# Optimization experiments

Measured on AMD Instinct MI355X. Metric: run time of the kernel, lower is better.

## Reference

```python
import jax, jax.numpy as jnp
import numpy as np

WS = 8          # window_size
POOL = 7        # int(sqrt(agent_num=49)) -> AdaptiveAvgPool1d output size


def _pool_matrix(L, p):
    """Averaging matrix [L, p] replicating torch AdaptiveAvgPool1d(L -> p)."""
    starts = np.floor(np.arange(p) * L / p).astype(int)
    ends = np.ceil((np.arange(p) + 1) * L / p).astype(int)
    P = np.zeros((L, p), dtype=np.float32)
    for i in range(p):
        P[starts[i]:ends[i], i] = 1.0 / (ends[i] - starts[i])
    return jnp.asarray(P)


def setup_inputs() -> dict:
    key = jax.random.key(0)
    ks = jax.random.split(key, 4)
    B, C, H, W = 8, 96, 192, 192
    s = 1.0 / np.sqrt(C)
    return {
        "x": jax.random.normal(ks[0], (B, C, H, W), jnp.float32),
        "Wv": jax.random.normal(ks[1], (C, C), jnp.float32) * s,
        "bv": jnp.zeros((C,), jnp.float32),
        "Wq": jax.random.normal(ks[2], (C, C), jnp.float32) * s,
        "bq": jnp.zeros((C,), jnp.float32),
        "Wk": jax.random.normal(ks[3], (C, C), jnp.float32) * s,
        "bk": jnp.zeros((C,), jnp.float32),
    }


def _conv1x1(x, Wt, b):
    # Conv2d(dim, dim, 1): weight [out, in]
    return jnp.einsum('bchw,oc->bohw', x, Wt) + b[None, :, None, None]


def reference(x, Wv, bv, Wq, bq, Wk, bk):
    B, C, H, W = x.shape
    ws = WS
    nh, nw = H // ws, W // ws
    L = ws * ws  # tokens per window (64)

    v = _conv1x1(x, Wv, bv)
    q = _conv1x1(x, Wq, bq)
    k = _conv1x1(x, Wk, bk)

    def win(t):  # b c (h dh) (w dw) -> (b h w) (dh dw) c
        t = t.reshape(B, C, nh, ws, nw, ws)
        return t.transpose(0, 2, 4, 3, 5, 1).reshape(B * nh * nw, L, C)

    vw, qw, kw = win(v), win(q), win(k)  # (N, 64, C) each

    # agent tokens: adaptive avg pool over the 64 in-window positions -> 7
    P = _pool_matrix(L, POOL)
    agent = jnp.einsum('nlc,lp->npc', qw, P)  # (N, 7, C)

    # agent attention (attn_drop = 0 -> identity)
    a_attn = jax.nn.softmax(jnp.einsum('npc,nlc->npl', agent, kw), axis=-1)
    agent_v = jnp.einsum('npl,nlc->npc', a_attn, vw)            # (N, 7, C)
    q_attn = jax.nn.softmax(jnp.einsum('nlc,npc->nlp', qw, agent), axis=-1)
    f = jnp.einsum('nlp,npc->nlc', q_attn, agent_v)             # (N, 64, C)

    # (b h w) (dh dw) c -> b c (h dh) (w dw)
    out = f.reshape(B, nh, nw, ws, ws, C).transpose(0, 5, 1, 3, 2, 4)
    return out.reshape(B, C, H, W)
```

## Files before the change

kernel.cpp:

```cpp
#include <hip/hip_runtime.h>


constexpr int C_   = 96;
constexpr int Wimg = 192;
constexpr int HWp  = 192 * 192;
constexpr int NWIN = 24;
constexpr int Pp   = 7;

typedef __attribute__((ext_vector_type(8))) __bf16 bf16x8;
typedef __attribute__((ext_vector_type(4))) __bf16 bf16x4;
typedef __attribute__((ext_vector_type(8))) short  short8;
typedef __attribute__((ext_vector_type(4))) float  f32x4;
union frag_u { short8 s; bf16x8 b; };

constexpr int XWS   = 0;
constexpr int XWLC  = 12288;
constexpr int R1    = 24768;
constexpr int R2    = 31168;
constexpr int QATB  = 37568;
constexpr int SMEMB = 39872;

constexpr int WS_FRAG_BYTE = 18944 * 4;
constexpr int WS_WV_BYTE   = WS_FRAG_BYTE + 84 * 1024;


__device__ __forceinline__ void bar() {
    asm volatile("s_waitcnt lgkmcnt(0)" ::: "memory");
    __builtin_amdgcn_s_barrier();
}

__device__ __forceinline__ void hilo8(const float4 a, const float4 b,
                                      frag_u& H, frag_u& L) {
    float v[8] = {a.x, a.y, a.z, a.w, b.x, b.y, b.z, b.w};
    #pragma unroll
    for (int j = 0; j < 8; ++j) {
        const __bf16 h = (__bf16)v[j];
        H.b[j] = h;
        L.b[j] = (__bf16)(v[j] - (float)h);
    }
}

__device__ __forceinline__ short8 xws_fragA(const unsigned char* S, int mt, int ks, int lane) {
    const int c  = mt * 16 + (lane & 15);
    const int l2 = ks * 64 + ((lane >> 4) << 4);
    return *reinterpret_cast<const short8*>(S + XWS + c * 128 + (l2 ^ ((c & 7) << 4)));
}


__global__ void precompute_mats(const float* __restrict__ Wq,
                                const float* __restrict__ Wk,
                                float* __restrict__ Mk,
                                float* __restrict__ Mq)
{
    const int c  = blockIdx.x;
    const int cp = threadIdx.x;
    float ak = 0.f, aq = 0.f;
    for (int a = 0; a < C_; ++a) {
        const float wq = Wq[a * C_ + c];
        ak = fmaf(wq, Wk[a * C_ + cp], ak);
        aq = fmaf(wq, Wq[a * C_ + cp], aq);
    }
    Mk[c * C_ + cp] = ak;
    Mq[c * C_ + cp] = aq;
}

__global__ void precompute_vecs(const float* __restrict__ Wq,
                                const float* __restrict__ Wk,
                                const float* __restrict__ bq,
                                const float* __restrict__ bk,
                                float* __restrict__ uk,  float* __restrict__ uq,
                                float* __restrict__ bk2, float* __restrict__ bq2,
                                float* __restrict__ scal)
{
    const int c = threadIdx.x;
    float a_uk = 0.f, a_uq = 0.f, a_bk2 = 0.f, a_bq2 = 0.f;
    for (int a = 0; a < C_; ++a) {
        const float wqc = Wq[a * C_ + c];
        a_uk  = fmaf(wqc, bk[a], a_uk);
        a_uq  = fmaf(wqc, bq[a], a_uq);
        a_bk2 = fmaf(bq[a], Wk[a * C_ + c], a_bk2);
        a_bq2 = fmaf(bq[a], Wq[a * C_ + c], a_bq2);
    }
    uk[c] = a_uk; uq[c] = a_uq; bk2[c] = a_bk2; bq2[c] = a_bq2;
    if (c == 0) {
        float sk = 0.f, sq = 0.f;
        for (int a = 0; a < C_; ++a) { sk += bq[a] * bk[a]; sq += bq[a] * bq[a]; }
        scal[0] = sk; scal[1] = sq;
    }
}

__global__ void precompute_frags(const float* __restrict__ ws,
                                 const float* __restrict__ Wv,
                                 unsigned char* __restrict__ wsb)
{
    const int bid = blockIdx.x, lane = threadIdx.x;
    short8 o;
    if (bid < 84) {
        const int hl = bid & 1, ks = (bid >> 1) % 3, nt = (bid / 6) % 7, mat = bid / 42;
        const float* M = ws + (mat ? 9216 : 0);
        const float* u = ws + (mat ? 18528 : 18432);
        const int col = nt * 16 + (lane & 15);
        #pragma unroll
        for (int j = 0; j < 8; ++j) {
            const int k = ks * 32 + (lane >> 4) * 8 + j;
            const float raw = (col < 96) ? M[k * 96 + col] : ((col == 96) ? u[k] : 0.f);
            const __bf16 hi = (__bf16)raw;
            union { __bf16 h; short s; } cv;
            cv.h = hl ? (__bf16)(raw - (float)hi) : hi;
            o[j] = cv.s;
        }
        *reinterpret_cast<short8*>(wsb + WS_FRAG_BYTE + bid * 1024 + lane * 16) = o;
    } else {
        const int wb = bid - 84;
        const int hl = wb & 1, ks = (wb >> 1) % 3, mt = wb / 6;
        const int row = mt * 16 + (lane & 15);
        #pragma unroll
        for (int j = 0; j < 8; ++j) {
            const int c = ks * 32 + (lane >> 4) * 8 + j;
            const float raw = Wv[row * 96 + c];
            const __bf16 hi = (__bf16)raw;
            union { __bf16 h; short s; } cv;
            cv.h = hl ? (__bf16)(raw - (float)hi) : hi;
            o[j] = cv.s;
        }
        *reinterpret_cast<short8*>(wsb + WS_WV_BYTE + wb * 1024 + lane * 16) = o;
    }
}

#define LOADPAIR(dstH, dstL, tab, slot_h) do {                                        \
    (dstH).s = *reinterpret_cast<const short8*>((tab) + (slot_h) * 1024 + (lane << 4));      \
    (dstL).s = *reinterpret_cast<const short8*>((tab) + ((slot_h) + 1) * 1024 + (lane << 4));\
} while (0)


__global__ __launch_bounds__(256, 4) void camixer_main(
    const float* __restrict__ x,
    const float* __restrict__ bv,
    const float* __restrict__ bk2,
    const float* __restrict__ bq2,
    const float* __restrict__ scal,
    const unsigned char* __restrict__ mfrag,
    const unsigned char* __restrict__ wvfrag,
    float* __restrict__ out)
{
    __shared__ __align__(16) unsigned char S[SMEMB];
    float* xpf  = (float*)(S + R1);
    float* Lraw = (float*)(S + R1);
    float* xvf  = (float*)(S + R1);
    float* gkq  = (float*)(S + R2);
    float* avT  = (float*)(S + R2);
    float* qat  = (float*)(S + QATB);

    const int t = threadIdx.x;
    const int lane = t & 63, w = t >> 6;
    const int wid = ((blockIdx.x & 7) * 576) + (blockIdx.x >> 3);
    const int b  = wid / (NWIN * NWIN);
    const int r  = wid % (NWIN * NWIN);
    const int h0 = (r / NWIN) * 8;
    const int w0 = (r % NWIN) * 8;
    const int base = b * C_ * HWp + h0 * Wimg + w0;
    const float scal0 = scal[0], scal1 = scal[1];

    frag_u B0h[3], B0l[3];
    LOADPAIR(B0h[0], B0l[0], mfrag, (w * 3 + 0) * 2);
    LOADPAIR(B0h[1], B0l[1], mfrag, (w * 3 + 1) * 2);
    LOADPAIR(B0h[2], B0l[2], mfrag, (w * 3 + 2) * 2);

    {
        const float4* x4 = reinterpret_cast<const float4*>(x);
        #pragma unroll
        for (int rr = 0; rr < 2; ++rr) {
            const int idx = t + (rr << 8);
            if (idx < 384) {
                const int dw4 = idx & 1;
                const int dh  = (idx >> 1) & 7;
                const int c4  = idx >> 4;
                const int c0 = c4 * 4, l0 = dh * 8 + dw4 * 4;
                __bf16 bf[4][4];
                #pragma unroll
                for (int j = 0; j < 4; ++j) {
                    const float4 v = x4[(base + (c0 + j) * HWp + dh * Wimg + dw4 * 4) >> 2];
                    bf[j][0] = (__bf16)v.x; bf[j][1] = (__bf16)v.y;
                    bf[j][2] = (__bf16)v.z; bf[j][3] = (__bf16)v.w;
                }
                #pragma unroll
                for (int j = 0; j < 4; ++j) {
                    const int c = c0 + j;
                    bf16x4 d = {bf[j][0], bf[j][1], bf[j][2], bf[j][3]};
                    *reinterpret_cast<bf16x4*>(S + XWS + c * 128 + ((l0 * 2) ^ ((c & 7) << 4))) = d;
                }
                #pragma unroll
                for (int i = 0; i < 4; ++i) {
                    const int l = l0 + i;
                    const int s = (c0 >> 5) * 4 + (l >> 4);
                    const int quad = (l & 15) + ((c0 >> 3) & 3) * 16;
                    bf16x4 d = {bf[0][i], bf[1][i], bf[2][i], bf[3][i]};
                    *reinterpret_cast<bf16x4*>(S + XWLC + s * 1040 + quad * 16 + (c0 & 7) * 2) = d;
                }
            }
        }
    }
    bar();

    {
        frag_u PAh[2], PAl[2];
        {
            const int p = lane & 15, kb = lane >> 4;
            const __bf16 PH = (__bf16)0.1f;
            const __bf16 PL = (__bf16)(0.1f - (float)PH);
            const int sp = (p < 7) ? ((p << 6) / 7) : 1000;
            #pragma unroll
            for (int ks = 0; ks < 2; ++ks)
                #pragma unroll
                for (int j = 0; j < 8; ++j) {
                    const int l = ks * 32 + kb * 8 + j;
                    const bool in = (l >= sp) && (l < sp + 10);
                    PAh[ks].b[j] = in ? PH : (__bf16)0.f;
                    PAl[ks].b[j] = in ? PL : (__bf16)0.f;
                }
        }
        #pragma unroll
        for (int rnd = 0; rnd < 2; ++rnd) {
            const int nt = rnd ? (4 + w) : w;
            if (rnd == 0 || w < 2) {
                f32x4 acc = {0.f, 0.f, 0.f, 0.f};
                #pragma unroll
                for (int ks = 0; ks < 2; ++ks) {
                    frag_u B;
                    B.s = xws_fragA(S, nt, ks, lane);
                    acc = __builtin_amdgcn_mfma_f32_16x16x32_bf16(PAh[ks].b, B.b, acc, 0, 0, 0);
                    acc = __builtin_amdgcn_mfma_f32_16x16x32_bf16(PAl[ks].b, B.b, acc, 0, 0, 0);
                }
                const int cc = nt * 16 + (lane & 15);
                #pragma unroll
                for (int rr = 0; rr < 4; ++rr)
                    xpf[((lane >> 4) * 4 + rr) * 100 + cc] = acc[rr];
            }
        }
    }
    bar();

    {
        frag_u Ah[3], Al[3];
        #pragma unroll
        for (int ks = 0; ks < 3; ++ks) {
            const int off = (lane & 15) * 100 + ks * 32 + (lane >> 4) * 8;
            hilo8(*reinterpret_cast<const float4*>(&xpf[off]),
                  *reinterpret_cast<const float4*>(&xpf[off + 4]), Ah[ks], Al[ks]);
        }

        #define G0TILE(TT, BH, BL) do {                                               \
            const int tt_ = (TT);                                                     \
            const int mat_ = (tt_ >= 7) ? 1 : 0;                                      \
            const int nt_  = tt_ - 7 * mat_;                                          \
            f32x4 acc = {0.f, 0.f, 0.f, 0.f};                                         \
            acc = __builtin_amdgcn_mfma_f32_16x16x32_bf16(Ah[0].b, BH[0].b, acc, 0,0,0); \
            acc = __builtin_amdgcn_mfma_f32_16x16x32_bf16(Ah[0].b, BL[0].b, acc, 0,0,0); \
            acc = __builtin_amdgcn_mfma_f32_16x16x32_bf16(Al[0].b, BH[0].b, acc, 0,0,0); \
            acc = __builtin_amdgcn_mfma_f32_16x16x32_bf16(Ah[1].b, BH[1].b, acc, 0,0,0); \
            acc = __builtin_amdgcn_mfma_f32_16x16x32_bf16(Ah[1].b, BL[1].b, acc, 0,0,0); \
            acc = __builtin_amdgcn_mfma_f32_16x16x32_bf16(Al[1].b, BH[1].b, acc, 0,0,0); \
            acc = __builtin_amdgcn_mfma_f32_16x16x32_bf16(Ah[2].b, BH[2].b, acc, 0,0,0); \
            acc = __builtin_amdgcn_mfma_f32_16x16x32_bf16(Ah[2].b, BL[2].b, acc, 0,0,0); \
            acc = __builtin_amdgcn_mfma_f32_16x16x32_bf16(Al[2].b, BH[2].b, acc, 0,0,0); \
            const int row0_ = (lane >> 4) * 4;                                        \
            if (nt_ < 6) {                                                            \
                const int cc_ = nt_ * 16 + (lane & 15);                               \
                const float b2v_ = (mat_ ? bq2 : bk2)[cc_];                           \
                _Pragma("unroll")                                                     \
                for (int rr = 0; rr < 4; ++rr) {                                      \
                    const int rw_ = row0_ + rr;                                       \
                    if (rw_ < 8) gkq[(rw_ + 8 * mat_) * 100 + cc_] = acc[rr] + b2v_;  \
                }                                                                     \
            } else if ((lane & 15) == 0) {                                            \
                _Pragma("unroll")                                                     \
                for (int rr = 0; rr < 4; ++rr) {                                      \
                    const int rw_ = row0_ + rr;                                       \
                    if (rw_ < 8) gkq[(rw_ + 8 * mat_) * 100 + 96] = acc[rr];          \
                }                                                                     \
            }                                                                         \
        } while (0)

        frag_u B1h[3], B1l[3], B2h[3], B2l[3], B3h[3], B3l[3];
        LOADPAIR(B1h[0], B1l[0], mfrag, (((w + 4) % 7 + 7 * ((w + 4) / 7)) * 3 + 0) * 2);
        LOADPAIR(B1h[1], B1l[1], mfrag, ((w + 4) * 3 + 1) * 2);
        LOADPAIR(B1h[2], B1l[2], mfrag, ((w + 4) * 3 + 2) * 2);
        G0TILE(w, B0h, B0l);
        LOADPAIR(B2h[0], B2l[0], mfrag, ((w + 8) * 3 + 0) * 2);
        LOADPAIR(B2h[1], B2l[1], mfrag, ((w + 8) * 3 + 1) * 2);
        LOADPAIR(B2h[2], B2l[2], mfrag, ((w + 8) * 3 + 2) * 2);
        G0TILE(w + 4, B1h, B1l);
        if (w < 2) {
            LOADPAIR(B3h[0], B3l[0], mfrag, ((w + 12) * 3 + 0) * 2);
            LOADPAIR(B3h[1], B3l[1], mfrag, ((w + 12) * 3 + 1) * 2);
            LOADPAIR(B3h[2], B3l[2], mfrag, ((w + 12) * 3 + 2) * 2);
        }
        G0TILE(w + 8, B2h, B2l);
        if (w < 2) G0TILE(w + 12, B3h, B3l);
        #undef G0TILE
    }
    bar();

    {
        frag_u B[3];
        #pragma unroll
        for (int ks = 0; ks < 3; ++ks)
            B[ks].s = *reinterpret_cast<const short8*>(S + XWLC + (ks * 4 + w) * 1040 + (lane << 4));
        frag_u Ah[3], Al[3];
        #pragma unroll
        for (int ks = 0; ks < 3; ++ks) {
            const int off = (lane & 15) * 100 + ks * 32 + (lane >> 4) * 8;
            hilo8(*reinterpret_cast<const float4*>(&gkq[off]),
                  *reinterpret_cast<const float4*>(&gkq[off + 4]), Ah[ks], Al[ks]);
        }
        f32x4 acc = {0.f, 0.f, 0.f, 0.f};
        #pragma unroll
        for (int ks = 0; ks < 3; ++ks) {
            acc = __builtin_amdgcn_mfma_f32_16x16x32_bf16(Ah[ks].b, B[ks].b, acc, 0, 0, 0);
            acc = __builtin_amdgcn_mfma_f32_16x16x32_bf16(Al[ks].b, B[ks].b, acc, 0, 0, 0);
        }
        const int colL = w * 16 + (lane & 15);
        #pragma unroll
        for (int rr = 0; rr < 4; ++rr) {
            const int pr = (lane >> 4) * 4 + rr;
            const float bias = gkq[pr * 100 + 96] + (pr < 8 ? scal0 : scal1);
            Lraw[pr * 66 + colL] = acc[rr] + bias;
        }
    }
    bar();

    if (w < 3) {
        #pragma unroll
        for (int rr = 0; rr < 2; ++rr) {
            const int pp = w + 3 * rr;
            const float v = Lraw[pp * 66 + lane];
            float mx = v;
            #pragma unroll
            for (int off = 32; off; off >>= 1) mx = fmaxf(mx, __shfl_xor(mx, off));
            const float e = __expf(v - mx);
            float s = e;
            #pragma unroll
            for (int off = 32; off; off >>= 1) s += __shfl_xor(s, off);
            const float a = e / s;
            const __bf16 hb = (__bf16)a;
            const __bf16 lb = (__bf16)(a - (float)hb);
            const int ks = lane >> 5;
            const int off_b = ((pp + 16 * ((lane >> 3) & 3)) << 4) + ((lane & 7) << 1);
            *reinterpret_cast<__bf16*>(S + R2 + (ks << 10) + off_b) = hb;
            *reinterpret_cast<__bf16*>(S + R2 + ((2 + ks) << 10) + off_b) = lb;
        }
    } else {
        {
            const int pp = 6;
            const float v = Lraw[pp * 66 + lane];
            float mx = v;
            #pragma unroll
            for (int off = 32; off; off >>= 1) mx = fmaxf(mx, __shfl_xor(mx, off));
            const float e = __expf(v - mx);
            float s = e;
            #pragma unroll
            for (int off = 32; off; off >>= 1) s += __shfl_xor(s, off);
            const float a = e / s;
            const __bf16 hb = (__bf16)a;
            const __bf16 lb = (__bf16)(a - (float)hb);
            const int ks = lane >> 5;
            const int off_b = ((pp + 16 * ((lane >> 3) & 3)) << 4) + ((lane & 7) << 1);
            *reinterpret_cast<__bf16*>(S + R2 + (ks << 10) + off_b) = hb;
            *reinterpret_cast<__bf16*>(S + R2 + ((2 + ks) << 10) + off_b) = lb;
        }
        float vv[Pp];
        float mx = -1e30f;
        #pragma unroll
        for (int p = 0; p < Pp; ++p) { vv[p] = Lraw[(8 + p) * 66 + lane]; mx = fmaxf(mx, vv[p]); }
        float s = 0.f;
        #pragma unroll
        for (int p = 0; p < Pp; ++p) { vv[p] = __expf(vv[p] - mx); s += vv[p]; }
        const float inv = 1.f / s;
        #pragma unroll
        for (int p = 0; p < Pp; ++p) qat[lane * 9 + p] = vv[p] * inv;
    }
    bar();

    frag_u V0h[3], V0l[3], V1h[3], V1l[3];
    {
        LOADPAIR(V0h[0], V0l[0], wvfrag, (w * 3 + 0) * 2);
        LOADPAIR(V0h[1], V0l[1], wvfrag, (w * 3 + 1) * 2);
        LOADPAIR(V0h[2], V0l[2], wvfrag, (w * 3 + 2) * 2);
        if (w < 2) {
            LOADPAIR(V1h[0], V1l[0], wvfrag, ((4 + w) * 3 + 0) * 2);
            LOADPAIR(V1h[1], V1l[1], wvfrag, ((4 + w) * 3 + 1) * 2);
            LOADPAIR(V1h[2], V1l[2], wvfrag, ((4 + w) * 3 + 2) * 2);
        }

        frag_u Bh[2], Bl[2];
        #pragma unroll
        for (int ks = 0; ks < 2; ++ks) {
            Bh[ks].s = *reinterpret_cast<const short8*>(S + R2 + (ks << 10) + (lane << 4));
            Bl[ks].s = *reinterpret_cast<const short8*>(S + R2 + ((2 + ks) << 10) + (lane << 4));
        }
        const int mt0 = (w < 2) ? w * 2 : (w + 2);
        const int nmt = (w < 2) ? 2 : 1;
        for (int m = 0; m < nmt; ++m) {
            const int mt = mt0 + m;
            f32x4 acc = {0.f, 0.f, 0.f, 0.f};
            #pragma unroll
            for (int ks = 0; ks < 2; ++ks) {
                frag_u A;
                A.s = xws_fragA(S, mt, ks, lane);
                acc = __builtin_amdgcn_mfma_f32_16x16x32_bf16(A.b, Bh[ks].b, acc, 0, 0, 0);
                acc = __builtin_amdgcn_mfma_f32_16x16x32_bf16(A.b, Bl[ks].b, acc, 0, 0, 0);
            }
            const int p = lane & 15;
            const int c0 = mt * 16 + (lane >> 4) * 4;
            *reinterpret_cast<f32x4*>(&xvf[p * 100 + c0]) = acc;
        }
    }
    bar();

    {
        frag_u Bh[3], Bl[3];
        #pragma unroll
        for (int ks = 0; ks < 3; ++ks) {
            const int off = (lane & 15) * 100 + ks * 32 + (lane >> 4) * 8;
            hilo8(*reinterpret_cast<const float4*>(&xvf[off]),
                  *reinterpret_cast<const float4*>(&xvf[off + 4]), Bh[ks], Bl[ks]);
        }
        #define G3TILE(MT, VH, VL) do {                                               \
            f32x4 acc = {0.f, 0.f, 0.f, 0.f};                                         \
            acc = __builtin_amdgcn_mfma_f32_16x16x32_bf16(VH[0].b, Bh[0].b, acc, 0,0,0); \
            acc = __builtin_amdgcn_mfma_f32_16x16x32_bf16(VH[0].b, Bl[0].b, acc, 0,0,0); \
            acc = __builtin_amdgcn_mfma_f32_16x16x32_bf16(VL[0].b, Bh[0].b, acc, 0,0,0); \
            acc = __builtin_amdgcn_mfma_f32_16x16x32_bf16(VH[1].b, Bh[1].b, acc, 0,0,0); \
            acc = __builtin_amdgcn_mfma_f32_16x16x32_bf16(VH[1].b, Bl[1].b, acc, 0,0,0); \
            acc = __builtin_amdgcn_mfma_f32_16x16x32_bf16(VL[1].b, Bh[1].b, acc, 0,0,0); \
            acc = __builtin_amdgcn_mfma_f32_16x16x32_bf16(VH[2].b, Bh[2].b, acc, 0,0,0); \
            acc = __builtin_amdgcn_mfma_f32_16x16x32_bf16(VH[2].b, Bl[2].b, acc, 0,0,0); \
            acc = __builtin_amdgcn_mfma_f32_16x16x32_bf16(VL[2].b, Bh[2].b, acc, 0,0,0); \
            if ((lane & 15) < 8) {                                                    \
                _Pragma("unroll")                                                     \
                for (int rr = 0; rr < 4; ++rr) {                                      \
                    const int o_ = (MT) * 16 + (lane >> 4) * 4 + rr;                  \
                    avT[o_ * 8 + (lane & 15)] = acc[rr] + bv[o_];                     \
                }                                                                     \
            }                                                                         \
        } while (0)
        G3TILE(w, V0h, V0l);
        if (w < 2) G3TILE(4 + w, V1h, V1l);
        #undef G3TILE
    }
    bar();

    {
        float qa[Pp];
        #pragma unroll
        for (int p = 0; p < Pp; ++p) qa[p] = qat[lane * 9 + p];
        const int dh = lane >> 3, dw = lane & 7;
        const int obase = b * C_ * HWp + (h0 + dh) * Wimg + (w0 + dw);
        #pragma unroll 4
        for (int j = 0; j < 24; ++j) {
            const int o = w + 4 * j;
            const float4 a0 = *reinterpret_cast<const float4*>(&avT[o * 8]);
            const float4 a1 = *reinterpret_cast<const float4*>(&avT[o * 8 + 4]);
            float acc = qa[0] * a0.x;
            acc = fmaf(qa[1], a0.y, acc);
            acc = fmaf(qa[2], a0.z, acc);
            acc = fmaf(qa[3], a0.w, acc);
            acc = fmaf(qa[4], a1.x, acc);
            acc = fmaf(qa[5], a1.y, acc);
            acc = fmaf(qa[6], a1.z, acc);
            out[obase + o * HWp] = acc;
        }
    }
}


extern "C" void kernel_launch(void* const* d_in, const int* in_sizes, int n_in,
                              void* d_out, int out_size, void* d_ws, size_t ws_size,
                              hipStream_t stream)
{
    const float* x  = (const float*)d_in[0];
    const float* Wv = (const float*)d_in[1];
    const float* bv = (const float*)d_in[2];
    const float* Wq = (const float*)d_in[3];
    const float* bq = (const float*)d_in[4];
    const float* Wk = (const float*)d_in[5];
    const float* bk = (const float*)d_in[6];
    float* out = (float*)d_out;

    float* ws = (float*)d_ws;
    float* Mk   = ws;
    float* Mq   = ws + 9216;
    float* uk   = ws + 18432;
    float* uq   = ws + 18528;
    float* bk2  = ws + 18624;
    float* bq2  = ws + 18720;
    float* scal = ws + 18816;
    unsigned char* wsb = (unsigned char*)d_ws;

    hipLaunchKernelGGL(precompute_mats, dim3(C_), dim3(C_), 0, stream,
                       Wq, Wk, Mk, Mq);
    hipLaunchKernelGGL(precompute_vecs, dim3(1), dim3(C_), 0, stream,
                       Wq, Wk, bq, bk, uk, uq, bk2, bq2, scal);
    hipLaunchKernelGGL(precompute_frags, dim3(120), dim3(64), 0, stream,
                       ws, Wv, wsb);
    hipLaunchKernelGGL(camixer_main, dim3(8 * NWIN * NWIN), dim3(256), 0, stream,
                       x, bv, bk2, bq2, scal,
                       wsb + WS_FRAG_BYTE, wsb + WS_WV_BYTE, out);
}
```

Baseline: 81.99 us.

## Store intermediates as bf16 hi/lo in LDS and run final contraction on MFMA

Intermediate tiles (pooled q, k/q projections, xv, agent-v) are now split into bf16 hi/lo pairs once, at write time into shared memory. Consumers then load ready-made MFMA fragments instead of reading fp32 and converting per lane. The final q_attn × agent_v contraction moves from scalar FMAs to bf16x3 MFMA with zero-padded K. The shared memory footprint shrinks slightly, which may allow higher occupancy. The cost is more scattered 2-byte LDS stores and some redundant zero-padded MFMA work.

New measurement: 78.27 us. 4.5% less time.

```diff
diff --git a/kernel.cpp b/kernel.cpp
--- a/kernel.cpp
+++ b/kernel.cpp
@@ -17,8 +17,12 @@
 constexpr int XWLC  = 12288;
 constexpr int R1    = 24768;
 constexpr int R2    = 31168;
-constexpr int QATB  = 37568;
-constexpr int SMEMB = 39872;
+constexpr int QATH  = XWLC;
+constexpr int QATL  = XWLC + 2560;
+constexpr int AVH   = R2;
+constexpr int AVL   = R2 + 3072;
+constexpr int BIAS  = 37568;
+constexpr int SMEMB = 37632;
 
 constexpr int WS_FRAG_BYTE = 18944 * 4;
 constexpr int WS_WV_BYTE   = WS_FRAG_BYTE + 84 * 1024;
@@ -27,23 +31,18 @@
 __device__ __forceinline__ void bar() {
     asm volatile("s_waitcnt lgkmcnt(0)" ::: "memory");
     __builtin_amdgcn_s_barrier();
-}
-
-__device__ __forceinline__ void hilo8(const float4 a, const float4 b,
-                                      frag_u& H, frag_u& L) {
-    float v[8] = {a.x, a.y, a.z, a.w, b.x, b.y, b.z, b.w};
-    #pragma unroll
-    for (int j = 0; j < 8; ++j) {
-        const __bf16 h = (__bf16)v[j];
-        H.b[j] = h;
-        L.b[j] = (__bf16)(v[j] - (float)h);
-    }
 }
 
 __device__ __forceinline__ short8 xws_fragA(const unsigned char* S, int mt, int ks, int lane) {
     const int c  = mt * 16 + (lane & 15);
     const int l2 = ks * 64 + ((lane >> 4) << 4);
     return *reinterpret_cast<const short8*>(S + XWS + c * 128 + (l2 ^ ((c & 7) << 4)));
+}
+
+__device__ __forceinline__ void put_hilo(unsigned char* S, int hi_off, int lo_off, float v) {
+    const __bf16 h = (__bf16)v;
+    *reinterpret_cast<__bf16*>(S + hi_off) = h;
+    *reinterpret_cast<__bf16*>(S + lo_off) = (__bf16)(v - (float)h);
 }
 
 
@@ -127,7 +126,7 @@
     }
 }
 
-#define LOADPAIR(dstH, dstL, tab, slot_h) do {                                        \
+#define LOADPAIR(dstH, dstL, tab, slot_h) do {                                               \
     (dstH).s = *reinterpret_cast<const short8*>((tab) + (slot_h) * 1024 + (lane << 4));      \
     (dstL).s = *reinterpret_cast<const short8*>((tab) + ((slot_h) + 1) * 1024 + (lane << 4));\
 } while (0)
@@ -144,12 +143,8 @@
     float* __restrict__ out)
 {
     __shared__ __align__(16) unsigned char S[SMEMB];
-    float* xpf  = (float*)(S + R1);
-    float* Lraw = (float*)(S + R1);
-    float* xvf  = (float*)(S + R1);
-    float* gkq  = (float*)(S + R2);
-    float* avT  = (float*)(S + R2);
-    float* qat  = (float*)(S + QATB);
+    float* Lraw   = (float*)(S + R1);
+    float* bias16 = (float*)(S + BIAS);
 
     const int t = threadIdx.x;
     const int lane = t & 63, w = t >> 6;
@@ -160,6 +155,7 @@
     const int w0 = (r % NWIN) * 8;
     const int base = b * C_ * HWp + h0 * Wimg + w0;
     const float scal0 = scal[0], scal1 = scal[1];
+    const short8 zero8 = {0, 0, 0, 0, 0, 0, 0, 0};
 
     frag_u B0h[3], B0l[3];
     LOADPAIR(B0h[0], B0l[0], mfrag, (w * 3 + 0) * 2);
@@ -205,7 +201,7 @@
     {
         frag_u PAh[2], PAl[2];
         {
-            const int p = lane & 15, kb = lane >> 4;
+            const int p = lane & 15;
             const __bf16 PH = (__bf16)0.1f;
             const __bf16 PL = (__bf16)(0.1f - (float)PH);
             const int sp = (p < 7) ? ((p << 6) / 7) : 1000;
@@ -213,7 +209,7 @@
             for (int ks = 0; ks < 2; ++ks)
                 #pragma unroll
                 for (int j = 0; j < 8; ++j) {
-                    const int l = ks * 32 + kb * 8 + j;
+                    const int l = ks * 32 + (lane >> 4) * 8 + j;
                     const bool in = (l >= sp) && (l < sp + 10);
                     PAh[ks].b[j] = in ? PH : (__bf16)0.f;
                     PAl[ks].b[j] = in ? PL : (__bf16)0.f;
@@ -233,8 +229,10 @@
                 }
                 const int cc = nt * 16 + (lane & 15);
                 #pragma unroll
-                for (int rr = 0; rr < 4; ++rr)
-                    xpf[((lane >> 4) * 4 + rr) * 100 + cc] = acc[rr];
+                for (int rr = 0; rr < 4; ++rr) {
+                    const int p = (lane >> 4) * 4 + rr;
+                    put_hilo(S, R1 + p * 200 + cc * 2, R1 + 3200 + p * 200 + cc * 2, acc[rr]);
+                }
             }
         }
     }
@@ -244,9 +242,9 @@
         frag_u Ah[3], Al[3];
         #pragma unroll
         for (int ks = 0; ks < 3; ++ks) {
-            const int off = (lane & 15) * 100 + ks * 32 + (lane >> 4) * 8;
-            hilo8(*reinterpret_cast<const float4*>(&xpf[off]),
-                  *reinterpret_cast<const float4*>(&xpf[off + 4]), Ah[ks], Al[ks]);
+            const int off = (lane & 15) * 200 + (ks * 32 + (lane >> 4) * 8) * 2;
+            Ah[ks].s = *reinterpret_cast<const short8*>(S + R1 + off);
+            Al[ks].s = *reinterpret_cast<const short8*>(S + R1 + 3200 + off);
         }
 
         #define G0TILE(TT, BH, BL) do {                                               \
@@ -270,19 +268,23 @@
                 _Pragma("unroll")                                                     \
                 for (int rr = 0; rr < 4; ++rr) {                                      \
                     const int rw_ = row0_ + rr;                                       \
-                    if (rw_ < 8) gkq[(rw_ + 8 * mat_) * 100 + cc_] = acc[rr] + b2v_;  \
+                    if (rw_ < 8) {                                                    \
+                        const int pr_ = rw_ + 8 * mat_;                               \
+                        put_hilo(S, R2 + pr_ * 200 + cc_ * 2,                         \
+                                 R2 + 3200 + pr_ * 200 + cc_ * 2, acc[rr] + b2v_);    \
+                    }                                                                 \
                 }                                                                     \
             } else if ((lane & 15) == 0) {                                            \
                 _Pragma("unroll")                                                     \
                 for (int rr = 0; rr < 4; ++rr) {                                      \
                     const int rw_ = row0_ + rr;                                       \
-                    if (rw_ < 8) gkq[(rw_ + 8 * mat_) * 100 + 96] = acc[rr];          \
+                    if (rw_ < 8) bias16[rw_ + 8 * mat_] = acc[rr];                    \
                 }                                                                     \
             }                                                                         \
         } while (0)
 
         frag_u B1h[3], B1l[3], B2h[3], B2l[3], B3h[3], B3l[3];
-        LOADPAIR(B1h[0], B1l[0], mfrag, (((w + 4) % 7 + 7 * ((w + 4) / 7)) * 3 + 0) * 2);
+        LOADPAIR(B1h[0], B1l[0], mfrag, ((w + 4) * 3 + 0) * 2);
         LOADPAIR(B1h[1], B1l[1], mfrag, ((w + 4) * 3 + 1) * 2);
         LOADPAIR(B1h[2], B1l[2], mfrag, ((w + 4) * 3 + 2) * 2);
         G0TILE(w, B0h, B0l);
@@ -309,9 +311,9 @@
         frag_u Ah[3], Al[3];
         #pragma unroll
         for (int ks = 0; ks < 3; ++ks) {
-            const int off = (lane & 15) * 100 + ks * 32 + (lane >> 4) * 8;
-            hilo8(*reinterpret_cast<const float4*>(&gkq[off]),
-                  *reinterpret_cast<const float4*>(&gkq[off + 4]), Ah[ks], Al[ks]);
+            const int off = (lane & 15) * 200 + (ks * 32 + (lane >> 4) * 8) * 2;
+            Ah[ks].s = *reinterpret_cast<const short8*>(S + R2 + off);
+            Al[ks].s = *reinterpret_cast<const short8*>(S + R2 + 3200 + off);
         }
         f32x4 acc = {0.f, 0.f, 0.f, 0.f};
         #pragma unroll
@@ -323,8 +325,7 @@
         #pragma unroll
         for (int rr = 0; rr < 4; ++rr) {
             const int pr = (lane >> 4) * 4 + rr;
-            const float bias = gkq[pr * 100 + 96] + (pr < 8 ? scal0 : scal1);
-            Lraw[pr * 66 + colL] = acc[rr] + bias;
+            Lraw[pr * 66 + colL] = acc[rr] + bias16[pr] + (pr < 8 ? scal0 : scal1);
         }
     }
     bar();
@@ -376,8 +377,18 @@
         #pragma unroll
         for (int p = 0; p < Pp; ++p) { vv[p] = __expf(vv[p] - mx); s += vv[p]; }
         const float inv = 1.f / s;
-        #pragma unroll
-        for (int p = 0; p < Pp; ++p) qat[lane * 9 + p] = vv[p] * inv;
+        frag_u qh, ql;
+        #pragma unroll
+        for (int p = 0; p < 8; ++p) {
+            const float a = (p < Pp) ? vv[p] * inv : 0.f;
+            const __bf16 hb = (__bf16)a;
+            qh.b[p] = hb;
+            ql.b[p] = (__bf16)(a - (float)hb);
+        }
+        *reinterpret_cast<short8*>(S + QATH + lane * 40)      = qh.s;
+        *reinterpret_cast<short8*>(S + QATH + lane * 40 + 16) = zero8;
+        *reinterpret_cast<short8*>(S + QATL + lane * 40)      = ql.s;
+        *reinterpret_cast<short8*>(S + QATL + lane * 40 + 16) = zero8;
     }
     bar();
 
@@ -411,19 +422,23 @@
                 acc = __builtin_amdgcn_mfma_f32_16x16x32_bf16(A.b, Bl[ks].b, acc, 0, 0, 0);
             }
             const int p = lane & 15;
-            const int c0 = mt * 16 + (lane >> 4) * 4;
-            *reinterpret_cast<f32x4*>(&xvf[p * 100 + c0]) = acc;
-        }
-    }
-    bar();
-
-    {
+            #pragma unroll
+            for (int rr = 0; rr < 4; ++rr) {
+                const int c = mt * 16 + (lane >> 4) * 4 + rr;
+                put_hilo(S, R1 + p * 200 + c * 2, R1 + 3200 + p * 200 + c * 2, acc[rr]);
+            }
+        }
+    }
+    bar();
+
+    {
+        const bool pok = (lane & 15) < Pp;
         frag_u Bh[3], Bl[3];
         #pragma unroll
         for (int ks = 0; ks < 3; ++ks) {
-            const int off = (lane & 15) * 100 + ks * 32 + (lane >> 4) * 8;
-            hilo8(*reinterpret_cast<const float4*>(&xvf[off]),
-                  *reinterpret_cast<const float4*>(&xvf[off + 4]), Bh[ks], Bl[ks]);
+            const int off = (lane & 15) * 200 + (ks * 32 + (lane >> 4) * 8) * 2;
+            Bh[ks].s = pok ? *reinterpret_cast<const short8*>(S + R1 + off)        : zero8;
+            Bl[ks].s = pok ? *reinterpret_cast<const short8*>(S + R1 + 3200 + off) : zero8;
         }
         #define G3TILE(MT, VH, VL) do {                                               \
             f32x4 acc = {0.f, 0.f, 0.f, 0.f};                                         \
@@ -436,12 +451,12 @@
             acc = __builtin_amdgcn_mfma_f32_16x16x32_bf16(VH[2].b, Bh[2].b, acc, 0,0,0); \
             acc = __builtin_amdgcn_mfma_f32_16x16x32_bf16(VH[2].b, Bl[2].b, acc, 0,0,0); \
             acc = __builtin_amdgcn_mfma_f32_16x16x32_bf16(VL[2].b, Bh[2].b, acc, 0,0,0); \
-            if ((lane & 15) < 8) {                                                    \
-                _Pragma("unroll")                                                     \
-                for (int rr = 0; rr < 4; ++rr) {                                      \
-                    const int o_ = (MT) * 16 + (lane >> 4) * 4 + rr;                  \
-                    avT[o_ * 8 + (lane & 15)] = acc[rr] + bv[o_];                     \
-                }                                                                     \
+            _Pragma("unroll")                                                         \
+            for (int rr = 0; rr < 4; ++rr) {                                          \
+                const int o_ = (MT) * 16 + (lane >> 4) * 4 + rr;                      \
+                const float v_ = acc[rr] + bv[o_];                                    \
+                put_hilo(S, AVH + o_ * 32 + (lane & 15) * 2,                          \
+                         AVL + o_ * 32 + (lane & 15) * 2, v_);                        \
             }                                                                         \
         } while (0)
         G3TILE(w, V0h, V0l);
@@ -451,24 +466,30 @@
     bar();
 
     {
-        float qa[Pp];
-        #pragma unroll
-        for (int p = 0; p < Pp; ++p) qa[p] = qat[lane * 9 + p];
-        const int dh = lane >> 3, dw = lane & 7;
-        const int obase = b * C_ * HWp + (h0 + dh) * Wimg + (w0 + dw);
-        #pragma unroll 4
-        for (int j = 0; j < 24; ++j) {
-            const int o = w + 4 * j;
-            const float4 a0 = *reinterpret_cast<const float4*>(&avT[o * 8]);
-            const float4 a1 = *reinterpret_cast<const float4*>(&avT[o * 8 + 4]);
-            float acc = qa[0] * a0.x;
-            acc = fmaf(qa[1], a0.y, acc);
-            acc = fmaf(qa[2], a0.z, acc);
-            acc = fmaf(qa[3], a0.w, acc);
-            acc = fmaf(qa[4], a1.x, acc);
-            acc = fmaf(qa[5], a1.y, acc);
-            acc = fmaf(qa[6], a1.z, acc);
-            out[obase + o * HWp] = acc;
+        const int kblk = lane >> 4, nlow = lane & 15;
+        const int l = w * 16 + nlow;
+        frag_u Bh, Bl;
+        if (kblk < 2) {
+            Bh.s = *reinterpret_cast<const short8*>(S + QATH + l * 40 + kblk * 16);
+            Bl.s = *reinterpret_cast<const short8*>(S + QATL + l * 40 + kblk * 16);
+        } else { Bh.s = zero8; Bl.s = zero8; }
+        const int obase = b * C_ * HWp + (h0 + (l >> 3)) * Wimg + w0 + (l & 7);
+        #pragma unroll
+        for (int mt = 0; mt < 6; ++mt) {
+            frag_u Ah, Al;
+            if (kblk < 2) {
+                Ah.s = *reinterpret_cast<const short8*>(S + AVH + (mt * 16 + nlow) * 32 + kblk * 16);
+                Al.s = *reinterpret_cast<const short8*>(S + AVL + (mt * 16 + nlow) * 32 + kblk * 16);
+            } else { Ah.s = zero8; Al.s = zero8; }
+            f32x4 acc = {0.f, 0.f, 0.f, 0.f};
+            acc = __builtin_amdgcn_mfma_f32_16x16x32_bf16(Ah.b, Bh.b, acc, 0, 0, 0);
+            acc = __builtin_amdgcn_mfma_f32_16x16x32_bf16(Ah.b, Bl.b, acc, 0, 0, 0);
+            acc = __builtin_amdgcn_mfma_f32_16x16x32_bf16(Al.b, Bh.b, acc, 0, 0, 0);
+            #pragma unroll
+            for (int rr = 0; rr < 4; ++rr) {
+                const int o = mt * 16 + kblk * 4 + rr;
+                out[obase + o * HWp] = acc[rr];
+            }
         }
     }
 }
```
